# Kernel optimization log

Measured on AMD Instinct MI355X. Metric: run time of the kernel, lower is better.

The kernel has to match this reference:

```python
import jax, jax.numpy as jnp
import numpy as np

N = 163842   # icosahedron level-7 vertices
CH = 64
EPS = 1e-5
SLOPE = 0.2

def _bn_lrelu(x, g, b):
    # BatchNorm1d over vertex dim (training-mode batch stats, biased var) + LeakyReLU(0.2)
    mu = jnp.mean(x, axis=0)
    var = jnp.var(x, axis=0)
    y = (x - mu) * jax.lax.rsqrt(var + EPS) * g + b
    return jnp.where(y > 0, y, SLOPE * y)

def _onering_conv(x, neigh, W, bias):
    # gather 7 one-ring neighbors per vertex, flatten, linear project
    n = x.shape[0]
    feat = x[neigh].reshape(n, -1)          # [N, 7*C]
    return feat @ W + bias                  # [N, out]

def setup_inputs() -> dict:
    key = jax.random.key(0)
    ks = jax.random.split(key, 8)
    d = {
        "x": jax.random.normal(ks[0], (N, CH), jnp.float32),
        "neigh_orders": jax.random.randint(ks[1], (7 * N,), 0, N, jnp.int64),
    }
    for i, k in enumerate([1, 2, 3, 4]):
        cin = CH * k
        d[f"g{k}"] = jnp.ones((cin,), jnp.float32)
        d[f"b{k}"] = jnp.zeros((cin,), jnp.float32)
        d[f"W{k}"] = jax.random.normal(ks[2 + i], (7 * cin, CH), jnp.float32) * (1.0 / np.sqrt(7 * cin))
        d[f"wb{k}"] = jnp.zeros((CH,), jnp.float32)
    return d

def reference(x, neigh_orders, g1, b1, g2, b2, g3, b3, g4, b4,
              W1, wb1, W2, wb2, W3, wb3, W4, wb4):
    x1 = _onering_conv(_bn_lrelu(x, g1, b1), neigh_orders, W1, wb1)
    c2 = jnp.concatenate((x, x1), axis=1)
    x2 = _onering_conv(_bn_lrelu(c2, g2, b2), neigh_orders, W2, wb2)
    c3 = jnp.concatenate((x, x1, x2), axis=1)
    x3 = _onering_conv(_bn_lrelu(c3, g3, b3), neigh_orders, W3, wb3)
    c4 = jnp.concatenate((x, x1, x2, x3), axis=1)
    x4 = _onering_conv(_bn_lrelu(c4, g4, b4), neigh_orders, W4, wb4)
    return x4
```

## Files before the change

### kernel.cpp

```cpp
#include <hip/hip_runtime.h>
#include <stdint.h>

#define NV 163842
#define EPSV 1e-5f

using short8 = __attribute__((ext_vector_type(8))) short;
using f32x4  = __attribute__((ext_vector_type(4))) float;

static __device__ __forceinline__ unsigned short f2bf(float f) {
    union { float f; unsigned int i; } v; v.f = f;
    return (unsigned short)((v.i + 0x7FFFu + ((v.i >> 16) & 1u)) >> 16);
}
static __device__ __forceinline__ void bf2x(unsigned int w, float& a, float& b) {
    union { unsigned int i; float f; } lo, hi;
    lo.i = w << 16; hi.i = w & 0xFFFF0000u;
    a = lo.f; b = hi.f;
}
static __device__ __forceinline__ unsigned int pack2(float a, float b) {
    union { float f; unsigned int i; } ua, ub; ua.f = a; ub.f = b;
    return __builtin_amdgcn_perm(ub.i + 0x8000u, ua.i + 0x8000u, 0x07060302);
}

__global__ __launch_bounds__(256) void k_zero(float* __restrict__ ACC) {
    ACC[threadIdx.x] = 0.f;
    ACC[256 + threadIdx.x] = 0.f;
}

__global__ __launch_bounds__(256) void k_cast(const float* __restrict__ x,
                                              unsigned short* __restrict__ C,
                                              float* __restrict__ ACC) {
    const int t = threadIdx.x;
    const int wv = t >> 6, lane = t & 63;
    const int v = blockIdx.x * 64 + (t >> 2);
    const int c0 = (t & 3) * 16;
    float f[16];
    const bool valid = v < NV;
    if (valid) {
        const float4* p = (const float4*)(x + (size_t)v * 64 + c0);
#pragma unroll
        for (int i = 0; i < 4; ++i) {
            float4 q = p[i];
            f[i * 4 + 0] = q.x; f[i * 4 + 1] = q.y; f[i * 4 + 2] = q.z; f[i * 4 + 3] = q.w;
        }
        unsigned int o[8];
#pragma unroll
        for (int i = 0; i < 8; ++i)
            o[i] = ((unsigned int)f2bf(f[2 * i])) | (((unsigned int)f2bf(f[2 * i + 1])) << 16);
        uint4* dst = (uint4*)(C + (size_t)v * 256 + c0);
        dst[0] = uint4{o[0], o[1], o[2], o[3]};
        dst[1] = uint4{o[4], o[5], o[6], o[7]};
    } else {
#pragma unroll
        for (int i = 0; i < 16; ++i) f[i] = 0.f;
    }
    float s[16], s2[16];
#pragma unroll
    for (int i = 0; i < 16; ++i) { s[i] = f[i]; s2[i] = f[i] * f[i]; }
#pragma unroll
    for (int mask = 4; mask <= 32; mask <<= 1) {
#pragma unroll
        for (int i = 0; i < 16; ++i) {
            s[i]  += __shfl_xor(s[i],  mask);
            s2[i] += __shfl_xor(s2[i], mask);
        }
    }
    __shared__ float red[4 * 128];
    if ((lane >> 2) == 0) {
        int cb = (lane & 3) * 16;
#pragma unroll
        for (int i = 0; i < 16; ++i) {
            red[wv * 128 + cb + i]      = s[i];
            red[wv * 128 + 64 + cb + i] = s2[i];
        }
    }
    __syncthreads();
    if (t < 128) {
        float v4 = red[t] + red[128 + t] + red[256 + t] + red[384 + t];
        int c = t & 63, which = t >> 6;
        atomicAdd(&ACC[which * 256 + c], v4);
    }
}

__global__ __launch_bounds__(256) void k_wt_all(const float* __restrict__ W1,
                                                const float* __restrict__ W2,
                                                const float* __restrict__ W3,
                                                const float* __restrict__ W4,
                                                unsigned short* __restrict__ WT) {
    int j = blockIdx.x * 256 + threadIdx.x;
    if (j >= 286720) return;
    const float* W; int jj, K7;
    if (j < 28672)       { W = W1; jj = j;          K7 = 448;  }
    else if (j < 86016)  { W = W2; jj = j - 28672;  K7 = 896;  }
    else if (j < 172032) { W = W3; jj = j - 86016;  K7 = 1344; }
    else                 { W = W4; jj = j - 172032; K7 = 1792; }
    int n = jj / K7, k = jj - n * K7;
    WT[j] = f2bf(W[(size_t)k * 64 + n]);
}

template<int CIN>
__global__ __launch_bounds__(256) void k_apply(const unsigned short* __restrict__ C,
                                               const float* __restrict__ ACC,
                                               const float* __restrict__ g,
                                               const float* __restrict__ bglob,
                                               unsigned short* __restrict__ Y) {
    __shared__ float ssc[CIN], ssh[CIN];
    const int t = threadIdx.x;
    if (t < CIN) {
        float s = ACC[t], s2 = ACC[256 + t];
        float mu = s * (1.0f / NV);
        float var = fmaf(-mu, mu, s2 * (1.0f / NV));
        float sc = g[t] * rsqrtf(var + EPSV);
        ssc[t] = sc;
        ssh[t] = bglob[t] - mu * sc;
    }
    __syncthreads();
    constexpr int C8 = CIN / 8;
    int e = blockIdx.x * 256 + t;
    if (e >= NV * C8) return;
    int v = e / C8, c8 = e - v * C8;
    int ch = c8 * 8;
    uint4 u = *(const uint4*)(C + (size_t)v * 256 + ch);
    float f[8];
    bf2x(u.x, f[0], f[1]); bf2x(u.y, f[2], f[3]);
    bf2x(u.z, f[4], f[5]); bf2x(u.w, f[6], f[7]);
    unsigned int o[4];
#pragma unroll
    for (int jj = 0; jj < 4; ++jj) {
        float y0 = fmaf(f[2 * jj],     ssc[ch + 2 * jj],     ssh[ch + 2 * jj]);
        float y1 = fmaf(f[2 * jj + 1], ssc[ch + 2 * jj + 1], ssh[ch + 2 * jj + 1]);
        y0 = y0 > 0.f ? y0 : 0.2f * y0;
        y1 = y1 > 0.f ? y1 : 0.2f * y1;
        o[jj] = pack2(y0, y1);
    }
    *(uint4*)(Y + (size_t)v * CIN + ch) = uint4{o[0], o[1], o[2], o[3]};
}

template<int CIN, int GRP, bool FINAL>
__global__ __launch_bounds__(512, 4) void k_gg(const unsigned short* __restrict__ Y,
                                               const int* __restrict__ neigh,
                                               const unsigned short* __restrict__ WT,
                                               const float* __restrict__ wb,
                                               float* __restrict__ ACC,
                                               unsigned short* __restrict__ Cout,
                                               float* __restrict__ Fout) {
    constexpr int KB2 = CIN / 32;
    constexpr int NC  = 7 * KB2;
    constexpr int NSEG = NC / 14;
    constexpr int K7  = 7 * CIN;

    __shared__ int sIdx[1792];
    __shared__ unsigned short sW[64 * 456];

    const int t = threadIdx.x;
    const int v0 = blockIdx.x * 256;

    for (int q = t; q < 1792; q += 512) {
        int gi = v0 * 7 + q;
        sIdx[q] = (gi < NV * 7) ? neigh[gi] : 0;
    }
    __syncthreads();

    const int wv = t >> 6, lane = t & 63;
    const int m = lane & 15, quad = lane >> 4;
    const int rb = wv * 32;
    const int qoff = quad * 8;

    int idx0[7], idx1[7];
#pragma unroll
    for (int r = 0; r < 7; ++r) {
        idx0[r] = sIdx[(rb + m) * 7 + r];
        idx1[r] = sIdx[(rb + 16 + m) * 7 + r];
    }

    f32x4 acc[2][4];
#pragma unroll
    for (int i = 0; i < 2; ++i)
#pragma unroll
        for (int j = 0; j < 4; ++j) acc[i][j] = f32x4{0.f, 0.f, 0.f, 0.f};

    auto loadA = [&](int c, short8& A0, short8& A1) {
        int r = c / KB2, kc = c - r * KB2;
        int ko = kc * 32 + qoff;
        A0 = *(const short8*)(Y + (size_t)idx0[r] * CIN + ko);
        A1 = *(const short8*)(Y + (size_t)idx1[r] * CIN + ko);
    };

    short8 a0[3], a1[3];
    loadA(0, a0[0], a1[0]);
    loadA(1, a0[1], a1[1]);
    loadA(2, a0[2], a1[2]);

#pragma unroll
    for (int seg = 0; seg < NSEG; ++seg) {
        __syncthreads();
        {
            const int n = wv * 8 + (lane >> 3);
            const int ch0 = lane & 7;
            const unsigned short* src = WT + (size_t)n * K7 + seg * 448;
            unsigned short* dst = sW + n * 456;
#pragma unroll
            for (int p = 0; p < 7; ++p) {
                int ch16 = p * 8 + ch0;
                *(uint4*)(dst + ch16 * 8) = *(const uint4*)(src + ch16 * 8);
            }
        }
        __syncthreads();
#pragma unroll
        for (int cc = 0; cc < 14; ++cc) {
            const int c = seg * 14 + cc;
            short8 na0, na1;
            if (c + 3 < NC) loadA(c + 3, na0, na1);
            const int buf = c % 3;
#pragma unroll
            for (int ct = 0; ct < 4; ++ct) {
                short8 bf = *(const short8*)(sW + (ct * 16 + m) * 456 + cc * 32 + qoff);
                acc[0][ct] = __builtin_amdgcn_mfma_f32_16x16x32_bf16(a0[buf], bf, acc[0][ct], 0, 0, 0);
                acc[1][ct] = __builtin_amdgcn_mfma_f32_16x16x32_bf16(a1[buf], bf, acc[1][ct], 0, 0, 0);
            }
            if (c + 3 < NC) { a0[buf] = na0; a1[buf] = na1; }
        }
    }

    __syncthreads();
    float bsum[4]  = {0.f, 0.f, 0.f, 0.f};
    float b2sum[4] = {0.f, 0.f, 0.f, 0.f};
#pragma unroll
    for (int mt = 0; mt < 2; ++mt) {
#pragma unroll
        for (int ct = 0; ct < 4; ++ct) {
            int col = ct * 16 + m;
            float bv = wb[col];
#pragma unroll
            for (int j = 0; j < 4; ++j) {
                int vr = v0 + wv * 32 + mt * 16 + quad * 4 + j;
                float val = acc[mt][ct][j] + bv;
                if (vr < NV) {
                    if (FINAL) {
                        Fout[(size_t)vr * 64 + col] = val;
                    } else {
                        Cout[(size_t)vr * 256 + GRP * 64 + col] = f2bf(val);
                        bsum[ct] += val; b2sum[ct] += val * val;
                    }
                }
            }
        }
    }
    if (!FINAL) {
#pragma unroll
        for (int ct = 0; ct < 4; ++ct) {
            bsum[ct]  += __shfl_xor(bsum[ct], 16);
            bsum[ct]  += __shfl_xor(bsum[ct], 32);
            b2sum[ct] += __shfl_xor(b2sum[ct], 16);
            b2sum[ct] += __shfl_xor(b2sum[ct], 32);
        }
        float* red = (float*)sW;
        if (quad == 0) {
#pragma unroll
            for (int ct = 0; ct < 4; ++ct) {
                red[wv * 128 + ct * 16 + m]        = bsum[ct];
                red[1024 + wv * 128 + ct * 16 + m] = b2sum[ct];
            }
        }
        __syncthreads();
        if (t < 128) {
            int c = t & 63, which = t >> 6;
            float s = 0.f;
#pragma unroll
            for (int w = 0; w < 8; ++w) s += red[which * 1024 + w * 128 + c];
            atomicAdd(&ACC[which * 256 + GRP * 64 + c], s);
        }
    }
}

extern "C" void kernel_launch(void* const* d_in, const int* in_sizes, int n_in,
                              void* d_out, int out_size, void* d_ws, size_t ws_size,
                              hipStream_t stream) {
    const float* x     = (const float*)d_in[0];
    const int*   neigh = (const int*)d_in[1];
    const float* G[4]  = {(const float*)d_in[2],  (const float*)d_in[6],
                          (const float*)d_in[10], (const float*)d_in[14]};
    const float* B[4]  = {(const float*)d_in[3],  (const float*)d_in[7],
                          (const float*)d_in[11], (const float*)d_in[15]};
    const float* W[4]  = {(const float*)d_in[4],  (const float*)d_in[8],
                          (const float*)d_in[12], (const float*)d_in[16]};
    const float* WB[4] = {(const float*)d_in[5],  (const float*)d_in[9],
                          (const float*)d_in[13], (const float*)d_in[17]};
    float* out = (float*)d_out;

    char* ws = (char*)d_ws;
    size_t off = 0;
    unsigned short* C  = (unsigned short*)(ws + off); off += (size_t)NV * 256 * 2;
    unsigned short* Yb = (unsigned short*)(ws + off); off += (size_t)NV * 256 * 2;
    unsigned short* WT = (unsigned short*)(ws + off); off += (size_t)286720 * 2;
    float* ACC         = (float*)(ws + off);          off += 512 * 4;

    k_zero<<<1, 256, 0, stream>>>(ACC);
    k_cast<<<(NV + 63) / 64, 256, 0, stream>>>(x, C, ACC);
    k_wt_all<<<(286720 + 255) / 256, 256, 0, stream>>>(W[0], W[1], W[2], W[3], WT);

    const int GG = (NV + 255) / 256;
#define APPLY(CIN, LI) k_apply<CIN><<<((NV * (CIN / 8)) + 255) / 256, 256, 0, stream>>>(C, ACC, G[LI], B[LI], Yb)
    APPLY(64, 0);
    k_gg< 64, 1, false><<<GG, 512, 0, stream>>>(Yb, neigh, WT,          WB[0], ACC, C, nullptr);
    APPLY(128, 1);
    k_gg<128, 2, false><<<GG, 512, 0, stream>>>(Yb, neigh, WT + 28672,  WB[1], ACC, C, nullptr);
    APPLY(192, 2);
    k_gg<192, 3, false><<<GG, 512, 0, stream>>>(Yb, neigh, WT + 86016,  WB[2], ACC, C, nullptr);
    APPLY(256, 3);
    k_gg<256, 0, true ><<<GG, 512, 0, stream>>>(Yb, neigh, WT + 172032, WB[3], ACC, nullptr, out);
#undef APPLY
}
```

Baseline: 561.7 us.

## Restructure gather-GEMM into small-tile register-prefetched weight streaming

Shrinks the gather-GEMM block from 512 to 256 threads and from 256 to 128 vertices. Instead of staging a large 448-wide weight segment in LDS, it streams a 64-column weight chunk per K step through registers into a small LDS tile. Each step prefetches the next gathered activation rows and weight chunk while running MFMAs on the current one. The goal is less LDS use and more resident blocks to hide gather latency, at the cost of two barriers per K-chunk and shallower prefetch. The LeakyReLU select also becomes an fmax.

Result: no change. 551.4 us (-1.8%).

```diff
diff --git a/kernel.cpp b/kernel.cpp
--- a/kernel.cpp
+++ b/kernel.cpp
@@ -128,33 +128,32 @@
     for (int jj = 0; jj < 4; ++jj) {
         float y0 = fmaf(f[2 * jj],     ssc[ch + 2 * jj],     ssh[ch + 2 * jj]);
         float y1 = fmaf(f[2 * jj + 1], ssc[ch + 2 * jj + 1], ssh[ch + 2 * jj + 1]);
-        y0 = y0 > 0.f ? y0 : 0.2f * y0;
-        y1 = y1 > 0.f ? y1 : 0.2f * y1;
+        y0 = fmaxf(y0, 0.2f * y0);
+        y1 = fmaxf(y1, 0.2f * y1);
         o[jj] = pack2(y0, y1);
     }
     *(uint4*)(Y + (size_t)v * CIN + ch) = uint4{o[0], o[1], o[2], o[3]};
 }
 
 template<int CIN, int GRP, bool FINAL>
-__global__ __launch_bounds__(512, 4) void k_gg(const unsigned short* __restrict__ Y,
+__global__ __launch_bounds__(256, 4) void k_gg(const unsigned short* __restrict__ Y,
                                                const int* __restrict__ neigh,
                                                const unsigned short* __restrict__ WT,
                                                const float* __restrict__ wb,
                                                float* __restrict__ ACC,
                                                unsigned short* __restrict__ Cout,
                                                float* __restrict__ Fout) {
-    constexpr int KB2 = CIN / 32;
-    constexpr int NC  = 7 * KB2;
-    constexpr int NSEG = NC / 14;
-    constexpr int K7  = 7 * CIN;
-
-    __shared__ int sIdx[1792];
-    __shared__ unsigned short sW[64 * 456];
+    constexpr int KB = CIN / 64;
+    constexpr int NC = 7 * KB;
+    constexpr int K7 = 7 * CIN;
+
+    __shared__ int sIdx[896];
+    __shared__ unsigned short sW[64 * 72];
 
     const int t = threadIdx.x;
-    const int v0 = blockIdx.x * 256;
-
-    for (int q = t; q < 1792; q += 512) {
+    const int v0 = blockIdx.x * 128;
+
+    for (int q = t; q < 896; q += 256) {
         int gi = v0 * 7 + q;
         sIdx[q] = (gi < NV * 7) ? neigh[gi] : 0;
     }
@@ -162,15 +161,15 @@
 
     const int wv = t >> 6, lane = t & 63;
     const int m = lane & 15, quad = lane >> 4;
-    const int rb = wv * 32;
-    const int qoff = quad * 8;
-
-    int idx0[7], idx1[7];
+    const int wrow = t >> 2, wq = t & 3;
+
+    unsigned int off0[7], off1[7];
 #pragma unroll
     for (int r = 0; r < 7; ++r) {
-        idx0[r] = sIdx[(rb + m) * 7 + r];
-        idx1[r] = sIdx[(rb + 16 + m) * 7 + r];
-    }
+        off0[r] = (unsigned)sIdx[(wv * 32 + m) * 7 + r] * (CIN * 2u);
+        off1[r] = (unsigned)sIdx[(wv * 32 + 16 + m) * 7 + r] * (CIN * 2u);
+    }
+    const char* Yb = (const char*)Y;
 
     f32x4 acc[2][4];
 #pragma unroll
@@ -178,50 +177,51 @@
 #pragma unroll
         for (int j = 0; j < 4; ++j) acc[i][j] = f32x4{0.f, 0.f, 0.f, 0.f};
 
-    auto loadA = [&](int c, short8& A0, short8& A1) {
-        int r = c / KB2, kc = c - r * KB2;
-        int ko = kc * 32 + qoff;
-        A0 = *(const short8*)(Y + (size_t)idx0[r] * CIN + ko);
-        A1 = *(const short8*)(Y + (size_t)idx1[r] * CIN + ko);
+    auto ldA = [&](int c, uint4* A0, uint4* A1) {
+        int r = c / KB, kc = c % KB;
+        const char* p0 = Yb + off0[r] + kc * 128 + quad * 16;
+        A0[0] = *(const uint4*)p0;
+        A0[1] = *(const uint4*)(p0 + 64);
+        const char* p1 = Yb + off1[r] + kc * 128 + quad * 16;
+        A1[0] = *(const uint4*)p1;
+        A1[1] = *(const uint4*)(p1 + 64);
     };
-
-    short8 a0[3], a1[3];
-    loadA(0, a0[0], a1[0]);
-    loadA(1, a0[1], a1[1]);
-    loadA(2, a0[2], a1[2]);
-
-#pragma unroll
-    for (int seg = 0; seg < NSEG; ++seg) {
+    auto ldW = [&](int c, uint4& W0, uint4& W1) {
+        const unsigned short* src = WT + (size_t)wrow * K7 + c * 64 + wq * 16;
+        W0 = *(const uint4*)src;
+        W1 = *(const uint4*)(src + 8);
+    };
+
+    uint4 a0[2], a1[2], w0, w1;
+    ldA(0, a0, a1);
+    ldW(0, w0, w1);
+
+#pragma unroll
+    for (int c = 0; c < NC; ++c) {
+        uint4 na0[2], na1[2], nw0, nw1;
+        if (c + 1 < NC) { ldA(c + 1, na0, na1); ldW(c + 1, nw0, nw1); }
+        *(uint4*)(sW + wrow * 72 + wq * 16)     = w0;
+        *(uint4*)(sW + wrow * 72 + wq * 16 + 8) = w1;
         __syncthreads();
-        {
-            const int n = wv * 8 + (lane >> 3);
-            const int ch0 = lane & 7;
-            const unsigned short* src = WT + (size_t)n * K7 + seg * 448;
-            unsigned short* dst = sW + n * 456;
-#pragma unroll
-            for (int p = 0; p < 7; ++p) {
-                int ch16 = p * 8 + ch0;
-                *(uint4*)(dst + ch16 * 8) = *(const uint4*)(src + ch16 * 8);
+#pragma unroll
+        for (int s = 0; s < 2; ++s) {
+            union { uint4 u; short8 s8; } ua, ub;
+            ua.u = a0[s]; ub.u = a1[s];
+#pragma unroll
+            for (int ct = 0; ct < 4; ++ct) {
+                short8 bf = *(const short8*)(sW + (ct * 16 + m) * 72 + s * 32 + quad * 8);
+                acc[0][ct] = __builtin_amdgcn_mfma_f32_16x16x32_bf16(ua.s8, bf, acc[0][ct], 0, 0, 0);
+                acc[1][ct] = __builtin_amdgcn_mfma_f32_16x16x32_bf16(ub.s8, bf, acc[1][ct], 0, 0, 0);
             }
         }
         __syncthreads();
-#pragma unroll
-        for (int cc = 0; cc < 14; ++cc) {
-            const int c = seg * 14 + cc;
-            short8 na0, na1;
-            if (c + 3 < NC) loadA(c + 3, na0, na1);
-            const int buf = c % 3;
-#pragma unroll
-            for (int ct = 0; ct < 4; ++ct) {
-                short8 bf = *(const short8*)(sW + (ct * 16 + m) * 456 + cc * 32 + qoff);
-                acc[0][ct] = __builtin_amdgcn_mfma_f32_16x16x32_bf16(a0[buf], bf, acc[0][ct], 0, 0, 0);
-                acc[1][ct] = __builtin_amdgcn_mfma_f32_16x16x32_bf16(a1[buf], bf, acc[1][ct], 0, 0, 0);
-            }
-            if (c + 3 < NC) { a0[buf] = na0; a1[buf] = na1; }
-        }
-    }
-
-    __syncthreads();
+        if (c + 1 < NC) {
+            a0[0] = na0[0]; a0[1] = na0[1];
+            a1[0] = na1[0]; a1[1] = na1[1];
+            w0 = nw0; w1 = nw1;
+        }
+    }
+
     float bsum[4]  = {0.f, 0.f, 0.f, 0.f};
     float b2sum[4] = {0.f, 0.f, 0.f, 0.f};
 #pragma unroll
@@ -254,19 +254,19 @@
             b2sum[ct] += __shfl_xor(b2sum[ct], 32);
         }
         float* red = (float*)sW;
+        __syncthreads();
         if (quad == 0) {
 #pragma unroll
             for (int ct = 0; ct < 4; ++ct) {
-                red[wv * 128 + ct * 16 + m]        = bsum[ct];
-                red[1024 + wv * 128 + ct * 16 + m] = b2sum[ct];
+                red[wv * 128 + ct * 16 + m]       = bsum[ct];
+                red[512 + wv * 128 + ct * 16 + m] = b2sum[ct];
             }
         }
         __syncthreads();
         if (t < 128) {
             int c = t & 63, which = t >> 6;
-            float s = 0.f;
-#pragma unroll
-            for (int w = 0; w < 8; ++w) s += red[which * 1024 + w * 128 + c];
+            float s = red[which * 512 + c] + red[which * 512 + 128 + c] +
+                      red[which * 512 + 256 + c] + red[which * 512 + 384 + c];
             atomicAdd(&ACC[which * 256 + GRP * 64 + c], s);
         }
     }
@@ -298,15 +298,16 @@
     k_cast<<<(NV + 63) / 64, 256, 0, stream>>>(x, C, ACC);
     k_wt_all<<<(286720 + 255) / 256, 256, 0, stream>>>(W[0], W[1], W[2], W[3], WT);
 
-    const int GG = (NV + 255) / 256;
+    const int GG = (NV + 127) / 128;
+    const int WOFF[4] = {0, 28672, 86016, 172032};
 #define APPLY(CIN, LI) k_apply<CIN><<<((NV * (CIN / 8)) + 255) / 256, 256, 0, stream>>>(C, ACC, G[LI], B[LI], Yb)
     APPLY(64, 0);
-    k_gg< 64, 1, false><<<GG, 512, 0, stream>>>(Yb, neigh, WT,          WB[0], ACC, C, nullptr);
+    k_gg< 64, 1, false><<<GG, 256, 0, stream>>>(Yb, neigh, WT + WOFF[0], WB[0], ACC, C, nullptr);
     APPLY(128, 1);
-    k_gg<128, 2, false><<<GG, 512, 0, stream>>>(Yb, neigh, WT + 28672,  WB[1], ACC, C, nullptr);
+    k_gg<128, 2, false><<<GG, 256, 0, stream>>>(Yb, neigh, WT + WOFF[1], WB[1], ACC, C, nullptr);
     APPLY(192, 2);
-    k_gg<192, 3, false><<<GG, 512, 0, stream>>>(Yb, neigh, WT + 86016,  WB[2], ACC, C, nullptr);
+    k_gg<192, 3, false><<<GG, 256, 0, stream>>>(Yb, neigh, WT + WOFF[2], WB[2], ACC, C, nullptr);
     APPLY(256, 3);
-    k_gg<256, 0, true ><<<GG, 512, 0, stream>>>(Yb, neigh, WT + 172032, WB[3], ACC, nullptr, out);
+    k_gg<256, 0, true ><<<GG, 256, 0, stream>>>(Yb, neigh, WT + WOFF[3], WB[3], ACC, nullptr, out);
 #undef APPLY
 }
```
